# Optimization experiments

Hardware: AMD Instinct MI355X
Metric: run time of the kernel (lower is better)

The kernel has to match this reference:

```python
import jax, jax.numpy as jnp
import numpy as np

D_MODEL = 2048
N_HEADS = 16
N_KV = 4
GROUP = N_HEADS // N_KV  # 4
D_K = D_MODEL // N_HEADS  # 128
D_V = D_MODEL // N_KV     # 512
THETA = 10000.0
Q_DIM = N_HEADS * D_K
K_DIM = N_KV * D_K
V_DIM = N_KV * D_V


def _apply_rope(t, sin, cos):
    # t: [B, H, L, D]; sin/cos: [L, D] broadcast over batch/heads
    half = t.shape[-1] // 2
    x1, x2 = t[..., :half], t[..., half:]
    rot = jnp.concatenate([-x2, x1], axis=-1)
    return t * cos + rot * sin


def setup_inputs() -> dict:
    key = jax.random.key(0)
    k1, k2, k3 = jax.random.split(key, 3)
    x = jax.random.normal(k1, (2, 2048, D_MODEL), dtype=jnp.float32)
    # attn_proj: Linear(d_model -> Q_DIM+K_DIM+V_DIM, bias=False); stored as [in, out]
    W_attn = jax.random.normal(k2, (D_MODEL, Q_DIM + K_DIM + V_DIM), dtype=jnp.float32) * 0.02
    # out_proj: Linear(n_heads*d_v -> d_model) with bias
    W_out = jax.random.normal(k3, (N_HEADS * D_V, D_MODEL), dtype=jnp.float32) * 0.02
    b_out = jnp.zeros((D_MODEL,), dtype=jnp.float32)
    return {"x": x, "W_attn": W_attn, "W_out": W_out, "b_out": b_out}


def reference(x, W_attn, W_out, b_out):
    B, L, _ = x.shape
    qkv = x @ W_attn  # [B, L, Q_DIM+K_DIM+V_DIM]
    q = qkv[..., :Q_DIM].reshape(B, L, N_HEADS, D_K).transpose(0, 2, 1, 3)          # [B,H,L,dk]
    k = qkv[..., Q_DIM:Q_DIM + K_DIM].reshape(B, L, N_KV, D_K).transpose(0, 2, 1, 3)  # [B,Hkv,L,dk]
    v = qkv[..., Q_DIM + K_DIM:].reshape(B, L, N_KV, D_V).transpose(0, 2, 1, 3)       # [B,Hkv,L,dv]

    # RoPE (computed in float32, as in source)
    inv_freq = 1.0 / (THETA ** (jnp.arange(0, D_K, 2, dtype=jnp.float32) / D_K))
    freqs = jnp.arange(L, dtype=jnp.float32)[:, None] * inv_freq[None, :]  # [L, dk/2]
    ang = jnp.concatenate([freqs, freqs], axis=-1)                          # [L, dk]
    sin, cos = jnp.sin(ang), jnp.cos(ang)
    q = _apply_rope(q.astype(jnp.float32), sin, cos).astype(x.dtype)
    k = _apply_rope(k.astype(jnp.float32), sin, cos).astype(x.dtype)

    # GQA: repeat_interleave(group, dim=1) is equivalent to grouping q heads as [kv, group]
    qg = q.reshape(B, N_KV, GROUP, L, D_K)
    scores = jnp.einsum('bkgqd,bkld->bkgql', qg, k) / (D_K ** 0.5)  # [B,Hkv,G,L,L]
    probs = jax.nn.softmax(scores, axis=-1)
    ctx = jnp.einsum('bkgql,bkle->bkgqe', probs, v)  # [B,Hkv,G,L,dv]
    ctx = ctx.reshape(B, N_HEADS, L, D_V).transpose(0, 2, 1, 3).reshape(B, L, N_HEADS * D_V)
    return ctx @ W_out + b_out
```

## Files before the change

### kernel.cpp

```cpp
#include <hip/hip_runtime.h>

typedef unsigned short u16;
typedef float f32x4 __attribute__((ext_vector_type(4)));
typedef __bf16 bf16x8 __attribute__((ext_vector_type(8)));

#define DEV static __device__ __forceinline__

DEV u16 f2bf(float f) {
  union { float f; unsigned u; } c; c.f = f;
  unsigned u = c.u;
  u += 0x7fffu + ((u >> 16) & 1u);
  return (u16)(u >> 16);
}
DEV float bf2f(u16 h) {
  union { float f; unsigned u; } c; c.u = ((unsigned)h) << 16;
  return c.f;
}
DEV f32x4 MFMA(bf16x8 a, bf16x8 b, f32x4 c) {
  return __builtin_amdgcn_mfma_f32_16x16x32_bf16(a, b, c, 0, 0, 0);
}
DEV unsigned cvt_pk_bf16(float a, float b) {
  unsigned r;
  asm("v_cvt_pk_bf16_f32 %0, %1, %2" : "=v"(r) : "v"(a), "v"(b));
  return r;
}
DEV float ex2(float x) { return __builtin_amdgcn_exp2f(x); }
DEV void glds16(const void* src, void* lds) {
  __builtin_amdgcn_global_load_lds(
      (__attribute__((address_space(1))) void*)src,
      (__attribute__((address_space(3))) void*)lds, 16, 0, 0);
}
DEV void barrier_raw() {
  __builtin_amdgcn_sched_barrier(0);
  asm volatile("s_barrier" ::: "memory");
  __builtin_amdgcn_sched_barrier(0);
}
#define VMCNT(N)                                              \
  do {                                                        \
    asm volatile("s_waitcnt vmcnt(" #N ")" ::: "memory");     \
    __builtin_amdgcn_sched_barrier(0);                        \
  } while (0)


__global__ void rope_tables(float* __restrict__ sinT, float* __restrict__ cosT) {
  int idx = blockIdx.x * 256 + threadIdx.x;
  int l = idx >> 6, i = idx & 63;
  float inv = __expf(-((float)(2 * i) / 128.0f) * 9.210340371976184f);
  float ang = (float)l * inv;
  sinT[idx] = sinf(ang);
  cosT[idx] = cosf(ang);
}

__global__ void cast_f32_bf16(const float* __restrict__ in, u16* __restrict__ out) {
  int i = (blockIdx.x * 256 + threadIdx.x) * 4;
  float4 v = *(const float4*)(in + i);
  ushort4 o;
  o.x = f2bf(v.x); o.y = f2bf(v.y); o.z = f2bf(v.z); o.w = f2bf(v.w);
  *(ushort4*)(out + i) = o;
}

__global__ void transpose_cast(const float* __restrict__ in, u16* __restrict__ out,
                               int R, int C) {
  __shared__ u16 tile[32][33];
  int c0 = blockIdx.x * 32, r0 = blockIdx.y * 32;
  int tx = threadIdx.x, ty = threadIdx.y;
  for (int i = 0; i < 32; i += 8)
    tile[ty + i][tx] = f2bf(in[(size_t)(r0 + ty + i) * C + c0 + tx]);
  __syncthreads();
  for (int i = 0; i < 32; i += 8)
    out[(size_t)(c0 + ty + i) * R + r0 + tx] = tile[tx][ty + i];
}

__global__ __launch_bounds__(512) void gemm1_8ph(const u16* __restrict__ A,
                                                 const u16* __restrict__ Bt,
                                                 u16* __restrict__ C) {
  constexpr int K = 2048, N = 4608, NT = 32;
  __shared__ __align__(16) u16 lA[2][2][8192];
  __shared__ __align__(16) u16 lB[2][2][8192];
  const int t = threadIdx.x, w = t >> 6, l = t & 63;
  const int lr = l & 15, lg = l >> 4;
  const int wr = w >> 2, wn = w & 3;
  const int swz = (blockIdx.x & 7) * 36 + (blockIdx.x >> 3);
  const int bm = swz & 15, bn = swz >> 4;

  const size_t aBase = (size_t)(bm * 256) * K;
  const size_t bBase = (size_t)(bn * 256) * K;
  const int lslog = (t & 3) ^ ((t >> 3) & 3);
  const int r128 = t >> 2;
  const int aswz = (lg ^ ((lr >> 1) & 3)) << 4;

  auto stA = [&](int buf, int kk, int tile) {
#pragma unroll
    for (int i = 0; i < 2; ++i) {
      int row = i * 128 + r128;
      glds16(A + aBase + (size_t)row * K + tile * 64 + kk * 32 + lslog * 8,
             &lA[buf][kk][i * 4096 + t * 8]);
    }
  };
  auto stB = [&](int buf, int kk, int tile) {
#pragma unroll
    for (int i = 0; i < 2; ++i) {
      int row = i * 128 + r128;
      glds16(Bt + bBase + (size_t)row * K + tile * 64 + kk * 32 + lslog * 8,
             &lB[buf][kk][i * 4096 + t * 8]);
    }
  };

  f32x4 acc[8][4];
#pragma unroll
  for (int f = 0; f < 8; ++f)
#pragma unroll
    for (int g = 0; g < 4; ++g) acc[f][g] = f32x4{0.f, 0.f, 0.f, 0.f};

  stA(0, 0, 0); stB(0, 0, 0); stA(0, 1, 0); stB(0, 1, 0); stA(1, 0, 1); stB(1, 0, 1);
  VMCNT(8);
  barrier_raw();

  auto PH = [&](int buf, int kk, int mh, auto&& st) {
    bf16x8 af[4], bb[4];
    const char* pA = (const char*)lA[buf][kk];
    const char* pB = (const char*)lB[buf][kk];
#pragma unroll
    for (int f = 0; f < 4; ++f) {
      af[f] = *(const bf16x8*)(pA + (wr * 128 + (mh * 4 + f) * 16 + lr) * 64 + aswz);
      bb[f] = *(const bf16x8*)(pB + (wn * 64 + f * 16 + lr) * 64 + aswz);
    }
    st();
    __builtin_amdgcn_s_setprio(1);
#pragma unroll
    for (int f = 0; f < 4; ++f)
#pragma unroll
      for (int g = 0; g < 4; ++g)
        acc[mh * 4 + f][g] = MFMA(af[f], bb[g], acc[mh * 4 + f][g]);
    __builtin_amdgcn_s_setprio(0);
  };
  auto NOST = [] {};

  for (int i = 0; i < NT / 2 - 1; ++i) {
    const int t1 = 2 * i + 1, t2 = 2 * i + 2, t3 = 2 * i + 3;
    PH(0, 0, 0, [&] { stA(1, 1, t1); });            barrier_raw();
    PH(0, 0, 1, [&] { stB(1, 1, t1); }); VMCNT(8);  barrier_raw();
    PH(0, 1, 0, [&] { stA(0, 0, t2); });            barrier_raw();
    PH(0, 1, 1, [&] { stB(0, 0, t2); }); VMCNT(8);  barrier_raw();
    PH(1, 0, 0, [&] { stA(0, 1, t2); });            barrier_raw();
    PH(1, 0, 1, [&] { stB(0, 1, t2); }); VMCNT(8);  barrier_raw();
    PH(1, 1, 0, [&] { stA(1, 0, t3); });            barrier_raw();
    PH(1, 1, 1, [&] { stB(1, 0, t3); }); VMCNT(8);  barrier_raw();
  }
  PH(0, 0, 0, [&] { stA(1, 1, NT - 1); });           barrier_raw();
  PH(0, 0, 1, [&] { stB(1, 1, NT - 1); }); VMCNT(8); barrier_raw();
  PH(0, 1, 0, NOST);                                 barrier_raw();
  PH(0, 1, 1, NOST);                       VMCNT(4); barrier_raw();
  PH(1, 0, 0, NOST);                                 barrier_raw();
  PH(1, 0, 1, NOST);                       VMCNT(0); barrier_raw();
  PH(1, 1, 0, NOST);                                 barrier_raw();
  PH(1, 1, 1, NOST);

  const int crow0 = bm * 256 + wr * 128;
  const int ccol0 = bn * 256 + wn * 64;
#pragma unroll
  for (int f = 0; f < 8; ++f)
#pragma unroll
    for (int g = 0; g < 4; ++g)
#pragma unroll
      for (int j = 0; j < 4; ++j)
        C[(size_t)(crow0 + f * 16 + lg * 4 + j) * N + ccol0 + g * 16 + lr] =
            f2bf(acc[f][g][j]);
}

__global__ __launch_bounds__(512) void gemm2_4ph(const u16* __restrict__ A,
                                                 const u16* __restrict__ Bt,
                                                 float* __restrict__ Cf,
                                                 const float* __restrict__ bias) {
  constexpr int K = 8192, N = 2048, NT = 128;
  __shared__ __align__(16) u16 lA[2][2][8192];
  __shared__ __align__(16) u16 lB[2][2][4096];
  const int t = threadIdx.x, w = t >> 6, l = t & 63;
  const int lr = l & 15, lg = l >> 4;
  const int wr = w >> 1, wn = w & 1;
  const int swz = (blockIdx.x & 7) * 32 + (blockIdx.x >> 3);
  const int bm = swz & 15, bn = swz >> 4;

  const size_t aBase = (size_t)(bm * 256) * K;
  const size_t bBase = (size_t)(bn * 128) * K;
  const int lslog = (t & 3) ^ ((t >> 3) & 3);
  const int r128 = t >> 2;
  const int aswz = (lg ^ ((lr >> 1) & 3)) << 4;

  auto stA = [&](int buf, int kk, int tile) {
#pragma unroll
    for (int i = 0; i < 2; ++i) {
      int row = i * 128 + r128;
      glds16(A + aBase + (size_t)row * K + tile * 64 + kk * 32 + lslog * 8,
             &lA[buf][kk][i * 4096 + t * 8]);
    }
  };
  auto stB = [&](int buf, int kk, int tile) {
    glds16(Bt + bBase + (size_t)r128 * K + tile * 64 + kk * 32 + lslog * 8,
           &lB[buf][kk][t * 8]);
  };

  f32x4 acc[4][4];
#pragma unroll
  for (int f = 0; f < 4; ++f)
#pragma unroll
    for (int g = 0; g < 4; ++g) acc[f][g] = f32x4{0.f, 0.f, 0.f, 0.f};

  stA(0, 0, 0); stB(0, 0, 0); stA(0, 1, 0); stB(0, 1, 0); stA(1, 0, 1); stB(1, 0, 1);
  VMCNT(6);
  barrier_raw();

  auto PH = [&](int buf, int kk, auto&& st) {
    bf16x8 af[4], bb[4];
    const char* pA = (const char*)lA[buf][kk];
    const char* pB = (const char*)lB[buf][kk];
#pragma unroll
    for (int f = 0; f < 4; ++f) {
      af[f] = *(const bf16x8*)(pA + (wr * 64 + f * 16 + lr) * 64 + aswz);
      bb[f] = *(const bf16x8*)(pB + (wn * 64 + f * 16 + lr) * 64 + aswz);
    }
    st();
    __builtin_amdgcn_s_setprio(1);
#pragma unroll
    for (int f = 0; f < 4; ++f)
#pragma unroll
      for (int g = 0; g < 4; ++g)
        acc[f][g] = MFMA(af[f], bb[g], acc[f][g]);
    __builtin_amdgcn_s_setprio(0);
  };
  auto NOST = [] {};

  for (int i = 0; i < NT / 2 - 1; ++i) {
    const int t1 = 2 * i + 1, t2 = 2 * i + 2, t3 = 2 * i + 3;
    PH(0, 0, [&] { stA(1, 1, t1); stB(1, 1, t1); }); VMCNT(6); barrier_raw();
    PH(0, 1, [&] { stA(0, 0, t2); stB(0, 0, t2); }); VMCNT(6); barrier_raw();
    PH(1, 0, [&] { stA(0, 1, t2); stB(0, 1, t2); }); VMCNT(6); barrier_raw();
    PH(1, 1, [&] { stA(1, 0, t3); stB(1, 0, t3); }); VMCNT(6); barrier_raw();
  }
  PH(0, 0, [&] { stA(1, 1, NT - 1); stB(1, 1, NT - 1); }); VMCNT(6); barrier_raw();
  PH(0, 1, NOST);                                          VMCNT(3); barrier_raw();
  PH(1, 0, NOST);                                          VMCNT(0); barrier_raw();
  PH(1, 1, NOST);

  const int crow0 = bm * 256 + wr * 64;
  const int ccol0 = bn * 128 + wn * 64;
#pragma unroll
  for (int g = 0; g < 4; ++g) {
    float bv = bias[ccol0 + g * 16 + lr];
#pragma unroll
    for (int f = 0; f < 4; ++f)
#pragma unroll
      for (int j = 0; j < 4; ++j)
        Cf[(size_t)(crow0 + f * 16 + lg * 4 + j) * N + ccol0 + g * 16 + lr] =
            acc[f][g][j] + bv;
  }
}

__global__ void rope_kernel(u16* __restrict__ qkv, const float* __restrict__ sinT,
                            const float* __restrict__ cosT) {
  int idx = blockIdx.x * 256 + threadIdx.x;
  int d = idx & 63;
  int rh = idx >> 6;
  int head = rh % 20;
  int row = rh / 20;
  int lpos = row & 2047;
  int col = head < 16 ? head * 128 : 2048 + (head - 16) * 128;
  float sc = head < 16 ? 0.12751743561938476f : 1.0f;
  u16* p = qkv + (size_t)row * 4608 + col;
  float x1 = bf2f(p[d]), x2 = bf2f(p[d + 64]);
  float c = cosT[lpos * 64 + d], s = sinT[lpos * 64 + d];
  p[d]      = f2bf((x1 * c - x2 * s) * sc);
  p[d + 64] = f2bf((x2 * c + x1 * s) * sc);
}

__global__ void vt_kernel(const u16* __restrict__ qkv, u16* __restrict__ vT) {
  __shared__ u16 tile[32][33];
  int bkv = blockIdx.z;
  int b = bkv >> 2, kv = bkv & 3;
  int e0 = blockIdx.x * 32, l0 = blockIdx.y * 32;
  const u16* src = qkv + (size_t)(b * 2048) * 4608 + 2560 + kv * 512;
  int tx = threadIdx.x, ty = threadIdx.y;
  for (int i = 0; i < 32; i += 8)
    tile[ty + i][tx] = src[(size_t)(l0 + ty + i) * 4608 + e0 + tx];
  __syncthreads();
  u16* dst = vT + (size_t)(bkv * 512) * 2048;
  int pi = ((tx >> 2) & 3) * 8 + ((tx >> 4) & 1) * 4 + (tx & 3);
  for (int i = 0; i < 32; i += 8)
    dst[(size_t)(e0 + ty + i) * 2048 + l0 + pi] = tile[tx][ty + i];
}

__global__ __launch_bounds__(512, 2) void attn_kernel(
    const u16* __restrict__ qkv, const u16* __restrict__ vT,
    u16* __restrict__ ctxb) {
  const int wg = blockIdx.x;
  const int pg = wg & 7, qt = wg >> 3;
  const int kvg = pg & 3, b = pg >> 2;
  const int t = threadIdx.x, w = t >> 6, l = t & 63;
  const int lr = l & 15, lg = l >> 4;
  const int h4 = w >> 1, eh = w & 1;
  const int h = kvg * 4 + h4;

  __shared__ __align__(16) u16 lK[2][32 * 128];
  __shared__ __align__(16) u16 lV[2][256 * 64];

  f32x4 zero = {0.f, 0.f, 0.f, 0.f};

  bf16x8 qf[2][4];
  const size_t qbase = (size_t)(b * 2048 + qt * 32);
#pragma unroll
  for (int m = 0; m < 2; ++m)
#pragma unroll
    for (int dc = 0; dc < 4; ++dc)
      qf[m][dc] = *(const bf16x8*)(qkv + (qbase + m * 16 + lr) * 4608 + h * 128 + dc * 32 + lg * 8);

  f32x4 acc[2][16];
#pragma unroll
  for (int m = 0; m < 2; ++m)
#pragma unroll
    for (int e = 0; e < 16; ++e) acc[m][e] = zero;
  float m_r[2] = {-1e30f, -1e30f};
  float l_r[2] = {0.f, 0.f};

  const size_t kbase = (size_t)(b * 2048) * 4608 + 2048 + kvg * 128;
  const size_t vbase = (size_t)((b * 4 + kvg) * 512) * 2048;

  const int krow = t >> 4;
  const int kp = t & 15;
  const int ks = (kp & 8) | ((kp ^ (krow & 7)) & 7);
  const u16* ksrc0 = qkv + kbase + (size_t)krow * 4608 + ks * 8;
  const int vs = (t & 7) ^ ((t >> 3) & 7);
  const int ve0 = (t >> 3) * 2 + (vs >> 2);
  const u16* vsrc0 = vT + vbase + (size_t)ve0 * 2048 + (vs & 3) * 8;

  const int vfoff = (eh * 128 + (lr >> 1)) * 128 +
                    (((((lr & 1) << 2) | lg) ^ ((lr >> 1) & 7)) << 4);

  auto stage = [&](int bi, int kv0) {
    glds16(ksrc0 + (size_t)kv0 * 4608, &lK[bi][t * 8]);
#pragma unroll
    for (int i = 0; i < 4; ++i)
      glds16(vsrc0 + kv0 + (size_t)i * 262144, &lV[bi][i * 4096 + t * 8]);
  };

  stage(0, 0);

  for (int it = 0; it < 64; ++it) {
    const int cur = it & 1;
    __syncthreads();
    if (it + 1 < 64) stage(cur ^ 1, 32 * (it + 1));
    const char* lKc = (const char*)lK[cur];
    const char* lVc = (const char*)lV[cur];

    f32x4 sT[2][2];
    sT[0][0] = zero; sT[0][1] = zero; sT[1][0] = zero; sT[1][1] = zero;
    __builtin_amdgcn_s_setprio(1);
#pragma unroll
    for (int dc = 0; dc < 4; ++dc) {
      int slot = dc * 4 + lg;
      int sw = (slot & 8) | ((slot ^ (lr & 7)) & 7);
#pragma unroll
      for (int kt = 0; kt < 2; ++kt) {
        bf16x8 kf = *(const bf16x8*)(lKc + (kt * 16 + lr) * 256 + sw * 16);
        sT[kt][0] = MFMA(kf, qf[0][dc], sT[kt][0]);
        sT[kt][1] = MFMA(kf, qf[1][dc], sT[kt][1]);
      }
    }
    __builtin_amdgcn_s_setprio(0);

    float lmax[2];
#pragma unroll
    for (int m = 0; m < 2; ++m) {
      float a0 = fmaxf(fmaxf(sT[0][m][0], sT[0][m][1]), fmaxf(sT[0][m][2], sT[0][m][3]));
      float a1 = fmaxf(fmaxf(sT[1][m][0], sT[1][m][1]), fmaxf(sT[1][m][2], sT[1][m][3]));
      lmax[m] = fmaxf(a0, a1);
    }
    bool need = (lmax[0] > m_r[0] + 11.5f) || (lmax[1] > m_r[1] + 11.5f);
    if (__any(need)) {
#pragma unroll
      for (int m = 0; m < 2; ++m) {
        float r = lmax[m];
        r = fmaxf(r, __shfl_xor(r, 16));
        r = fmaxf(r, __shfl_xor(r, 32));
        float mn = fmaxf(m_r[m], r);
        float al = ex2(m_r[m] - mn);
        m_r[m] = mn; l_r[m] *= al;
        float alj[4];
#pragma unroll
        for (int j = 0; j < 4; ++j) alj[j] = __shfl(al, lg * 4 + j);
#pragma unroll
        for (int e = 0; e < 16; ++e)
#pragma unroll
          for (int j = 0; j < 4; ++j) acc[m][e][j] *= alj[j];
      }
    }

    bf16x8 pf[2];
#pragma unroll
    for (int m = 0; m < 2; ++m) {
      float p0 = ex2(sT[0][m][0] - m_r[m]), p1 = ex2(sT[0][m][1] - m_r[m]);
      float p2 = ex2(sT[0][m][2] - m_r[m]), p3 = ex2(sT[0][m][3] - m_r[m]);
      float p4 = ex2(sT[1][m][0] - m_r[m]), p5 = ex2(sT[1][m][1] - m_r[m]);
      float p6 = ex2(sT[1][m][2] - m_r[m]), p7 = ex2(sT[1][m][3] - m_r[m]);
      l_r[m] += ((p0 + p1) + (p2 + p3)) + ((p4 + p5) + (p6 + p7));
      union { bf16x8 v; unsigned wd[4]; } u;
      u.wd[0] = cvt_pk_bf16(p0, p1);
      u.wd[1] = cvt_pk_bf16(p2, p3);
      u.wd[2] = cvt_pk_bf16(p4, p5);
      u.wd[3] = cvt_pk_bf16(p6, p7);
      pf[m] = u.v;
    }

    __builtin_amdgcn_s_setprio(1);
#pragma unroll
    for (int e = 0; e < 16; ++e) {
      bf16x8 vf = *(const bf16x8*)(lVc + vfoff + e * 1024);
      acc[0][e] = MFMA(pf[0], vf, acc[0][e]);
      acc[1][e] = MFMA(pf[1], vf, acc[1][e]);
    }
    __builtin_amdgcn_s_setprio(0);
  }

#pragma unroll
  for (int m = 0; m < 2; ++m) {
    float s = l_r[m];
    s += __shfl_xor(s, 16);
    s += __shfl_xor(s, 32);
    l_r[m] = s;
  }
#pragma unroll
  for (int m = 0; m < 2; ++m) {
    float linv[4];
#pragma unroll
    for (int j = 0; j < 4; ++j) linv[j] = 1.0f / __shfl(l_r[m], lg * 4 + j);
    const size_t orow0 = qbase + m * 16 + lg * 4;
#pragma unroll
    for (int e = 0; e < 16; ++e)
#pragma unroll
      for (int j = 0; j < 4; ++j)
        ctxb[(orow0 + j) * 8192 + h * 512 + eh * 256 + e * 16 + lr] =
            f2bf(acc[m][e][j] * linv[j]);
  }
}

extern "C" void kernel_launch(void* const* d_in, const int* in_sizes, int n_in,
                              void* d_out, int out_size, void* d_ws, size_t ws_size,
                              hipStream_t stream) {
  const float* x      = (const float*)d_in[0];
  const float* W_attn = (const float*)d_in[1];
  const float* W_out  = (const float*)d_in[2];
  const float* b_out  = (const float*)d_in[3];
  float* out = (float*)d_out;
  char* ws = (char*)d_ws;

  if (ws_size < 158334976u) return;

  float* sinT = (float*)(ws + 0);
  float* cosT = (float*)(ws + 524288);
  u16* xb   = (u16*)(ws + 1048576);
  u16* WbT  = (u16*)(ws + 17825792);
  u16* qkvb = (u16*)(ws + 36700160);
  u16* vT   = (u16*)(ws + 74448896);
  u16* ctxb = (u16*)(ws + 91226112);
  u16* WobT = (u16*)(ws + 1048576);

  rope_tables<<<512, 256, 0, stream>>>(sinT, cosT);
  cast_f32_bf16<<<8192, 256, 0, stream>>>(x, xb);
  transpose_cast<<<dim3(144, 64), dim3(32, 8), 0, stream>>>(W_attn, WbT, 2048, 4608);
  gemm1_8ph<<<288, 512, 0, stream>>>(xb, WbT, qkvb);
  rope_kernel<<<20480, 256, 0, stream>>>(qkvb, sinT, cosT);
  vt_kernel<<<dim3(16, 64, 8), dim3(32, 8), 0, stream>>>(qkvb, vT);
  attn_kernel<<<512, 512, 0, stream>>>(qkvb, vT, ctxb);
  transpose_cast<<<dim3(64, 256), dim3(32, 8), 0, stream>>>(W_out, WobT, 8192, 2048);
  gemm2_4ph<<<256, 512, 0, stream>>>(ctxb, WobT, out, b_out);
}
```

Measured before the change: 585.3 us.

## Stage 64-key tiles per barrier in attention and fuse small prep kernels

The attention loop now loads 64 keys and values per double-buffered stage and runs two 32-key compute halves between barriers, halving the number of barriers and stage issues. Separately, the rope-table, x-cast and W_attn transpose kernels are merged into one launch, and rope and the V transpose are merged into another, cutting launch overhead. The larger attention buffers raise LDS use to about 160KB per workgroup. That likely drops residency from the two workgroups per CU requested by launch bounds to one, reducing latency hiding.

```diff
diff --git a/kernel.cpp b/kernel.cpp
--- a/kernel.cpp
+++ b/kernel.cpp
@@ -42,21 +42,34 @@
   } while (0)
 
 
-__global__ void rope_tables(float* __restrict__ sinT, float* __restrict__ cosT) {
-  int idx = blockIdx.x * 256 + threadIdx.x;
-  int l = idx >> 6, i = idx & 63;
-  float inv = __expf(-((float)(2 * i) / 128.0f) * 9.210340371976184f);
-  float ang = (float)l * inv;
-  sinT[idx] = sinf(ang);
-  cosT[idx] = cosf(ang);
-}
-
-__global__ void cast_f32_bf16(const float* __restrict__ in, u16* __restrict__ out) {
-  int i = (blockIdx.x * 256 + threadIdx.x) * 4;
-  float4 v = *(const float4*)(in + i);
-  ushort4 o;
-  o.x = f2bf(v.x); o.y = f2bf(v.y); o.z = f2bf(v.z); o.w = f2bf(v.w);
-  *(ushort4*)(out + i) = o;
+__global__ void prep_kernel(const float* __restrict__ x, const float* __restrict__ W_attn,
+                            float* __restrict__ sinT, float* __restrict__ cosT,
+                            u16* __restrict__ xb, u16* __restrict__ WbT) {
+  __shared__ u16 tile[32][33];
+  const int bk = blockIdx.x, t = threadIdx.x;
+  if (bk < 512) {
+    int idx = bk * 256 + t;
+    int l = idx >> 6, i = idx & 63;
+    float inv = __expf(-((float)(2 * i) / 128.0f) * 9.210340371976184f);
+    float ang = (float)l * inv;
+    sinT[idx] = sinf(ang);
+    cosT[idx] = cosf(ang);
+  } else if (bk < 8704) {
+    int i = ((bk - 512) * 256 + t) * 4;
+    float4 v = *(const float4*)(x + i);
+    ushort4 o;
+    o.x = f2bf(v.x); o.y = f2bf(v.y); o.z = f2bf(v.z); o.w = f2bf(v.w);
+    *(ushort4*)(xb + i) = o;
+  } else {
+    int idx = bk - 8704;
+    int c0 = (idx % 144) * 32, r0 = (idx / 144) * 32;
+    int tx = t & 31, ty = t >> 5;
+    for (int i = 0; i < 32; i += 8)
+      tile[ty + i][tx] = f2bf(W_attn[(size_t)(r0 + ty + i) * 4608 + c0 + tx]);
+    __syncthreads();
+    for (int i = 0; i < 32; i += 8)
+      WbT[(size_t)(c0 + ty + i) * 2048 + r0 + tx] = tile[tx][ty + i];
+  }
 }
 
 __global__ void transpose_cast(const float* __restrict__ in, u16* __restrict__ out,
@@ -256,37 +269,39 @@
   }
 }
 
-__global__ void rope_kernel(u16* __restrict__ qkv, const float* __restrict__ sinT,
-                            const float* __restrict__ cosT) {
-  int idx = blockIdx.x * 256 + threadIdx.x;
-  int d = idx & 63;
-  int rh = idx >> 6;
-  int head = rh % 20;
-  int row = rh / 20;
-  int lpos = row & 2047;
-  int col = head < 16 ? head * 128 : 2048 + (head - 16) * 128;
-  float sc = head < 16 ? 0.12751743561938476f : 1.0f;
-  u16* p = qkv + (size_t)row * 4608 + col;
-  float x1 = bf2f(p[d]), x2 = bf2f(p[d + 64]);
-  float c = cosT[lpos * 64 + d], s = sinT[lpos * 64 + d];
-  p[d]      = f2bf((x1 * c - x2 * s) * sc);
-  p[d + 64] = f2bf((x2 * c + x1 * s) * sc);
-}
-
-__global__ void vt_kernel(const u16* __restrict__ qkv, u16* __restrict__ vT) {
+__global__ void ropevt_kernel(u16* __restrict__ qkv, const float* __restrict__ sinT,
+                              const float* __restrict__ cosT, u16* __restrict__ vT) {
   __shared__ u16 tile[32][33];
-  int bkv = blockIdx.z;
-  int b = bkv >> 2, kv = bkv & 3;
-  int e0 = blockIdx.x * 32, l0 = blockIdx.y * 32;
-  const u16* src = qkv + (size_t)(b * 2048) * 4608 + 2560 + kv * 512;
-  int tx = threadIdx.x, ty = threadIdx.y;
-  for (int i = 0; i < 32; i += 8)
-    tile[ty + i][tx] = src[(size_t)(l0 + ty + i) * 4608 + e0 + tx];
-  __syncthreads();
-  u16* dst = vT + (size_t)(bkv * 512) * 2048;
-  int pi = ((tx >> 2) & 3) * 8 + ((tx >> 4) & 1) * 4 + (tx & 3);
-  for (int i = 0; i < 32; i += 8)
-    dst[(size_t)(e0 + ty + i) * 2048 + l0 + pi] = tile[tx][ty + i];
+  const int bk = blockIdx.x, t = threadIdx.x;
+  if (bk < 20480) {
+    int idx = bk * 256 + t;
+    int d = idx & 63;
+    int rh = idx >> 6;
+    int head = rh % 20;
+    int row = rh / 20;
+    int lpos = row & 2047;
+    int col = head < 16 ? head * 128 : 2048 + (head - 16) * 128;
+    float sc = head < 16 ? 0.12751743561938476f : 1.0f;
+    u16* p = qkv + (size_t)row * 4608 + col;
+    float x1 = bf2f(p[d]), x2 = bf2f(p[d + 64]);
+    float c = cosT[lpos * 64 + d], s = sinT[lpos * 64 + d];
+    p[d]      = f2bf((x1 * c - x2 * s) * sc);
+    p[d + 64] = f2bf((x2 * c + x1 * s) * sc);
+  } else {
+    int idx = bk - 20480;
+    int bx = idx & 15, by = (idx >> 4) & 63, bkv = idx >> 10;
+    int b = bkv >> 2, kv = bkv & 3;
+    int e0 = bx * 32, l0 = by * 32;
+    const u16* src = qkv + (size_t)(b * 2048) * 4608 + 2560 + kv * 512;
+    int tx = t & 31, ty = t >> 5;
+    for (int i = 0; i < 32; i += 8)
+      tile[ty + i][tx] = src[(size_t)(l0 + ty + i) * 4608 + e0 + tx];
+    __syncthreads();
+    u16* dst = vT + (size_t)(bkv * 512) * 2048;
+    int pi = ((tx >> 2) & 3) * 8 + ((tx >> 4) & 1) * 4 + (tx & 3);
+    for (int i = 0; i < 32; i += 8)
+      dst[(size_t)(e0 + ty + i) * 2048 + l0 + pi] = tile[tx][ty + i];
+  }
 }
 
 __global__ __launch_bounds__(512, 2) void attn_kernel(
@@ -300,8 +315,8 @@
   const int h4 = w >> 1, eh = w & 1;
   const int h = kvg * 4 + h4;
 
-  __shared__ __align__(16) u16 lK[2][32 * 128];
-  __shared__ __align__(16) u16 lV[2][256 * 64];
+  __shared__ __align__(16) u16 lK[2][64 * 128];
+  __shared__ __align__(16) u16 lV[2][512 * 64];
 
   f32x4 zero = {0.f, 0.f, 0.f, 0.f};
 
@@ -336,21 +351,20 @@
                     (((((lr & 1) << 2) | lg) ^ ((lr >> 1) & 7)) << 4);
 
   auto stage = [&](int bi, int kv0) {
-    glds16(ksrc0 + (size_t)kv0 * 4608, &lK[bi][t * 8]);
-#pragma unroll
-    for (int i = 0; i < 4; ++i)
-      glds16(vsrc0 + kv0 + (size_t)i * 262144, &lV[bi][i * 4096 + t * 8]);
+#pragma unroll
+    for (int i = 0; i < 2; ++i)
+      glds16(ksrc0 + (size_t)(kv0 + i * 32) * 4608, &lK[bi][i * 4096 + t * 8]);
+#pragma unroll
+    for (int hh = 0; hh < 2; ++hh)
+#pragma unroll
+      for (int i = 0; i < 4; ++i)
+        glds16(vsrc0 + (kv0 + hh * 32) + (size_t)i * 262144,
+               &lV[bi][hh * 16384 + i * 4096 + t * 8]);
   };
 
   stage(0, 0);
 
-  for (int it = 0; it < 64; ++it) {
-    const int cur = it & 1;
-    __syncthreads();
-    if (it + 1 < 64) stage(cur ^ 1, 32 * (it + 1));
-    const char* lKc = (const char*)lK[cur];
-    const char* lVc = (const char*)lV[cur];
-
+  auto half_body = [&](const char* lKc, const char* lVc) {
     f32x4 sT[2][2];
     sT[0][0] = zero; sT[0][1] = zero; sT[1][0] = zero; sT[1][1] = zero;
     __builtin_amdgcn_s_setprio(1);
@@ -418,6 +432,16 @@
       acc[1][e] = MFMA(pf[1], vf, acc[1][e]);
     }
     __builtin_amdgcn_s_setprio(0);
+  };
+
+  for (int it = 0; it < 32; ++it) {
+    const int cur = it & 1;
+    __syncthreads();
+    if (it + 1 < 32) stage(cur ^ 1, 64 * (it + 1));
+    const char* lKc = (const char*)lK[cur];
+    const char* lVc = (const char*)lV[cur];
+    half_body(lKc, lVc);
+    half_body(lKc + 8192, lVc + 32768);
   }
 
 #pragma unroll
@@ -463,12 +487,9 @@
   u16* ctxb = (u16*)(ws + 91226112);
   u16* WobT = (u16*)(ws + 1048576);
 
-  rope_tables<<<512, 256, 0, stream>>>(sinT, cosT);
-  cast_f32_bf16<<<8192, 256, 0, stream>>>(x, xb);
-  transpose_cast<<<dim3(144, 64), dim3(32, 8), 0, stream>>>(W_attn, WbT, 2048, 4608);
+  prep_kernel<<<17920, 256, 0, stream>>>(x, W_attn, sinT, cosT, xb, WbT);
   gemm1_8ph<<<288, 512, 0, stream>>>(xb, WbT, qkvb);
-  rope_kernel<<<20480, 256, 0, stream>>>(qkvb, sinT, cosT);
-  vt_kernel<<<dim3(16, 64, 8), dim3(32, 8), 0, stream>>>(qkvb, vT);
+  ropevt_kernel<<<28672, 256, 0, stream>>>(qkvb, sinT, cosT, vT);
   attn_kernel<<<512, 512, 0, stream>>>(qkvb, vT, ctxb);
   transpose_cast<<<dim3(64, 256), dim3(32, 8), 0, stream>>>(W_out, WobT, 8192, 2048);
   gemm2_4ph<<<256, 512, 0, stream>>>(ctxb, WobT, out, b_out);
```

Result: faster. 557.8 us (-4.7%).
